# Kernel optimization log

Measured on AMD Instinct MI355X. Metric: run time of the kernel, lower is better.

The kernel has to match this reference:

```python
import jax, jax.numpy as jnp
import numpy as np

N = 100000
D = 100
E = 1600000


def setup_inputs() -> dict:
    key = jax.random.key(0)
    k1, k2, k3, k4 = jax.random.split(key, 4)
    embedding = jax.random.normal(k1, (N, D), dtype=jnp.float32)
    adj_rows = jax.random.randint(k2, (E,), 0, N, dtype=jnp.int32)
    adj_cols = jax.random.randint(k3, (E,), 0, N, dtype=jnp.int32)
    adj_vals = jax.random.uniform(k4, (E,), dtype=jnp.float32)
    return {
        "embedding": embedding,
        "adj_rows": adj_rows,
        "adj_cols": adj_cols,
        "adj_vals": adj_vals,
        "layer_num": 3,
    }


def _spmm(rows, cols, vals, x):
    # sparse [N,N] @ dense [N,D] via gather + weighted segment-sum scatter
    msgs = x[cols] * vals[:, None]           # [E, D]
    return jax.ops.segment_sum(msgs, rows, num_segments=N)  # [N, D]


def reference(embedding, adj_rows, adj_cols, adj_vals, layer_num):
    # out = sum_{i=0}^{layer_num} A^i x  (accumulate hops, including layer 0)
    h = embedding
    acc = embedding
    for _ in range(layer_num):
        h = _spmm(adj_rows, adj_cols, adj_vals, h)
        acc = acc + h
    return acc
```

## Files before the change

kernel.cpp:

```cpp
#include <hip/hip_runtime.h>


#define NODES 100000
#define DIM 100
#define DIM4 25
#define CH 16
#define BSHIFT 8
#define NBUCKETS ((NODES + 255) >> 8)
#define NPAD (NBUCKETS << BSHIFT)

typedef _Float16 half4_t __attribute__((ext_vector_type(4)));
typedef _Float16 half8_t __attribute__((ext_vector_type(8)));

__global__ void cvt_hist_kernel(const float4* __restrict__ emb, half4_t* __restrict__ x0,
                                const int* __restrict__ rows, int* __restrict__ bktCount, int E) {
    __shared__ int h[NBUCKETS];
    for (int i = threadIdx.x; i < NBUCKETS; i += blockDim.x) h[i] = 0;
    __syncthreads();
    int stride = gridDim.x * blockDim.x;
    int gid = blockIdx.x * blockDim.x + threadIdx.x;
    for (int i = gid; i < NODES * 32; i += stride) {
        int r = i >> 5, c = i & 31;
        half4_t hv;
        if (c < 25) {
            float4 f = emb[r * 25 + c];
            hv.x = (_Float16)f.x; hv.y = (_Float16)f.y;
            hv.z = (_Float16)f.z; hv.w = (_Float16)f.w;
        } else {
            hv.x = (_Float16)0.f; hv.y = (_Float16)0.f;
            hv.z = (_Float16)0.f; hv.w = (_Float16)0.f;
        }
        x0[i] = hv;
    }
    for (int e = gid; e < E; e += stride)
        atomicAdd(&h[rows[e] >> BSHIFT], 1);
    __syncthreads();
    for (int i = threadIdx.x; i < NBUCKETS; i += blockDim.x)
        if (h[i]) atomicAdd(&bktCount[i], h[i]);
}

__global__ void pass1_kernel(const int* __restrict__ rows, const int* __restrict__ cols,
                             const float* __restrict__ vals,
                             const int* __restrict__ bktCount, int* __restrict__ gCur,
                             int* __restrict__ bktStart,
                             int2* __restrict__ staging, int E) {
    __shared__ int cnt[NBUCKETS];
    __shared__ int bst[NBUCKETS];
    __shared__ int sc[512];
    int t = threadIdx.x;
    for (int i = t; i < NBUCKETS; i += 512) cnt[i] = 0;
    __syncthreads();
    int chunk = (E + gridDim.x - 1) / gridDim.x;
    int s = blockIdx.x * chunk;
    int e = min(E, s + chunk);
    for (int i = s + t; i < e; i += 512)
        atomicAdd(&cnt[rows[i] >> BSHIFT], 1);
    int v = (t < NBUCKETS) ? bktCount[t] : 0;
    sc[t] = v;
    __syncthreads();
    for (int off = 1; off < 512; off <<= 1) {
        int x = (t >= off) ? sc[t - off] : 0;
        __syncthreads();
        sc[t] += x;
        __syncthreads();
    }
    int excl = sc[t] - v;
    if (blockIdx.x == 0) {
        if (t < NBUCKETS) bktStart[t] = excl;
        if (t == 0) bktStart[NBUCKETS] = E;
    }
    if (t < NBUCKETS) {
        int c = cnt[t];
        bst[t] = excl + (c ? atomicAdd(&gCur[t], c) : 0);
        cnt[t] = 0;
    }
    __syncthreads();
    for (int i = s + t; i < e; i += 512) {
        int r = rows[i];
        int b = r >> BSHIFT;
        int pos = bst[b] + atomicAdd(&cnt[b], 1);
        staging[pos] = make_int2(cols[i] | ((r & 255) << 17), __float_as_int(vals[i]));
    }
}

__global__ void pass2_kernel(const int* __restrict__ bktStart, const int2* __restrict__ staging,
                             int* __restrict__ rowstart, int2* __restrict__ csr) {
    __shared__ int hist[256];
    __shared__ int cur[256];
    int b = blockIdx.x, t = threadIdx.x;
    int s = bktStart[b], e = bktStart[b + 1];
    if (t < 256) hist[t] = 0;
    __syncthreads();
    for (int i = s + t; i < e; i += 512)
        atomicAdd(&hist[(staging[i].x >> 17) & 255], 1);
    __syncthreads();
    int v = (t < 256) ? hist[t] : 0;
    if (t < 256) cur[t] = v;
    __syncthreads();
    for (int off = 1; off < 256; off <<= 1) {
        int x = (t >= off && t < 256) ? cur[t - off] : 0;
        __syncthreads();
        if (t < 256) cur[t] += x;
        __syncthreads();
    }
    if (t < 256) {
        int excl = cur[t] - v;
        rowstart[(b << BSHIFT) + t] = s + excl;
        hist[t] = excl;
    }
    __syncthreads();
    for (int i = s + t; i < e; i += 512) {
        int2 rec = staging[i];
        int lr = (rec.x >> 17) & 255;
        int p = atomicAdd(&hist[lr], 1);
        csr[s + p] = make_int2(rec.x & 0x1FFFF, rec.y);
    }
}

__global__ void gather_mid4_kernel(const int* __restrict__ rowstart,
                                   const int2* __restrict__ csr,
                                   const half8_t* __restrict__ x,
                                   half8_t* __restrict__ h) {
    int gid = blockIdx.x * blockDim.x + threadIdx.x;
    int row = gid >> 4, lane = gid & 15;
    if (row >= NODES) return;
    int s = rowstart[row], e = rowstart[row + 1];
    float acc[8] = {0.f, 0.f, 0.f, 0.f, 0.f, 0.f, 0.f, 0.f};
    int i = s;
    for (; i + 3 < e; i += 4) {
        int2 r0 = csr[i], r1 = csr[i + 1], r2 = csr[i + 2], r3 = csr[i + 3];
        half8_t a0 = x[((size_t)r0.x << 4) + lane];
        half8_t a1 = x[((size_t)r1.x << 4) + lane];
        half8_t a2 = x[((size_t)r2.x << 4) + lane];
        half8_t a3 = x[((size_t)r3.x << 4) + lane];
        float v0 = __int_as_float(r0.y), v1 = __int_as_float(r1.y);
        float v2 = __int_as_float(r2.y), v3 = __int_as_float(r3.y);
        #pragma unroll
        for (int k = 0; k < 8; ++k)
            acc[k] += v0 * (float)a0[k] + v1 * (float)a1[k]
                    + v2 * (float)a2[k] + v3 * (float)a3[k];
    }
    for (; i < e; ++i) {
        int2 r0 = csr[i];
        half8_t a0 = x[((size_t)r0.x << 4) + lane];
        float v0 = __int_as_float(r0.y);
        #pragma unroll
        for (int k = 0; k < 8; ++k) acc[k] += v0 * (float)a0[k];
    }
    half8_t hv;
    #pragma unroll
    for (int k = 0; k < 8; ++k) hv[k] = (_Float16)acc[k];
    h[((size_t)row << 4) + lane] = hv;
}

__global__ void gather_mid8_kernel(const int* __restrict__ rowstart,
                                   const int2* __restrict__ csr,
                                   const half8_t* __restrict__ x,
                                   half8_t* __restrict__ h) {
    int gid = blockIdx.x * blockDim.x + threadIdx.x;
    int row = gid >> 4, lane = gid & 15;
    if (row >= NODES) return;
    int s = rowstart[row], e = rowstart[row + 1];
    float acc[8] = {0.f, 0.f, 0.f, 0.f, 0.f, 0.f, 0.f, 0.f};
    int i = s;
    for (; i + 7 < e; i += 8) {
        int2 rr[8];
        #pragma unroll
        for (int j = 0; j < 8; ++j) rr[j] = csr[i + j];
        half8_t aa[8];
        #pragma unroll
        for (int j = 0; j < 8; ++j) aa[j] = x[((size_t)rr[j].x << 4) + lane];
        #pragma unroll
        for (int j = 0; j < 8; ++j) {
            float v = __int_as_float(rr[j].y);
            #pragma unroll
            for (int k = 0; k < 8; ++k) acc[k] += v * (float)aa[j][k];
        }
    }
    for (; i < e; ++i) {
        int2 r0 = csr[i];
        half8_t a0 = x[((size_t)r0.x << 4) + lane];
        float v0 = __int_as_float(r0.y);
        #pragma unroll
        for (int k = 0; k < 8; ++k) acc[k] += v0 * (float)a0[k];
    }
    half8_t hv;
    #pragma unroll
    for (int k = 0; k < 8; ++k) hv[k] = (_Float16)acc[k];
    h[((size_t)row << 4) + lane] = hv;
}

__global__ void gather_last_kernel(const int* __restrict__ rowstart,
                                   const int2* __restrict__ csr,
                                   const half8_t* __restrict__ x,
                                   const half8_t* __restrict__ x0,
                                   const half8_t* __restrict__ h1,
                                   const half8_t* __restrict__ h2,
                                   float4* __restrict__ out) {
    int gid = blockIdx.x * blockDim.x + threadIdx.x;
    int row = gid >> 4, lane = gid & 15;
    if (row >= NODES) return;
    int s = rowstart[row], e = rowstart[row + 1];
    float acc[8] = {0.f, 0.f, 0.f, 0.f, 0.f, 0.f, 0.f, 0.f};
    int i = s;
    for (; i + 7 < e; i += 8) {
        int2 rr[8];
        #pragma unroll
        for (int j = 0; j < 8; ++j) rr[j] = csr[i + j];
        half8_t aa[8];
        #pragma unroll
        for (int j = 0; j < 8; ++j) aa[j] = x[((size_t)rr[j].x << 4) + lane];
        #pragma unroll
        for (int j = 0; j < 8; ++j) {
            float v = __int_as_float(rr[j].y);
            #pragma unroll
            for (int k = 0; k < 8; ++k) acc[k] += v * (float)aa[j][k];
        }
    }
    for (; i < e; ++i) {
        int2 r0 = csr[i];
        half8_t a0 = x[((size_t)r0.x << 4) + lane];
        float v0 = __int_as_float(r0.y);
        #pragma unroll
        for (int k = 0; k < 8; ++k) acc[k] += v0 * (float)a0[k];
    }
    size_t pidx = ((size_t)row << 4) + lane;
    half8_t xe = x0[pidx], a1 = h1[pidx], a2 = h2[pidx];
    int f4 = row * DIM4 + lane * 2;
    if (lane < 13) {
        float4 o0;
        o0.x = acc[0] + (float)xe[0] + (float)a1[0] + (float)a2[0];
        o0.y = acc[1] + (float)xe[1] + (float)a1[1] + (float)a2[1];
        o0.z = acc[2] + (float)xe[2] + (float)a1[2] + (float)a2[2];
        o0.w = acc[3] + (float)xe[3] + (float)a1[3] + (float)a2[3];
        out[f4] = o0;
    }
    if (lane < 12) {
        float4 o1;
        o1.x = acc[4] + (float)xe[4] + (float)a1[4] + (float)a2[4];
        o1.y = acc[5] + (float)xe[5] + (float)a1[5] + (float)a2[5];
        o1.z = acc[6] + (float)xe[6] + (float)a1[6] + (float)a2[6];
        o1.w = acc[7] + (float)xe[7] + (float)a1[7] + (float)a2[7];
        out[f4 + 1] = o1;
    }
}

extern "C" void kernel_launch(void* const* d_in, const int* in_sizes, int n_in,
                              void* d_out, int out_size, void* d_ws, size_t ws_size,
                              hipStream_t stream) {
    const float* emb  = (const float*)d_in[0];
    const int*   rows = (const int*)  d_in[1];
    const int*   cols = (const int*)  d_in[2];
    const float* vals = (const float*)d_in[3];
    const int E = in_sizes[1];

    const size_t ndp_bytes = (size_t)NODES * 128 * sizeof(_Float16);

    char* w = (char*)d_ws;
    half8_t* x0p      = (half8_t*)w;  w += ndp_bytes;
    half8_t* h1p      = (half8_t*)w;  w += ndp_bytes;
    half8_t* h2p      = (half8_t*)w;  w += ndp_bytes;
    int2*    staging  = (int2*)h2p;
    int2*    csr      = (int2*)   w;  w += (size_t)E * sizeof(int2);
    int*     rowstart = (int*)    w;  w += (size_t)(NPAD + 256) * sizeof(int);
    int*     bktCount = (int*)    w;  w += 512 * sizeof(int);
    int*     gCur     = (int*)    w;  w += 512 * sizeof(int);
    int*     bktStart = (int*)    w;  w += 512 * sizeof(int);

    float4* out = (float4*)d_out;

    hipMemsetAsync(bktCount, 0, 1024 * sizeof(int), stream);
    cvt_hist_kernel<<<1024, 256, 0, stream>>>((const float4*)emb, (half4_t*)x0p,
                                              rows, bktCount, E);
    pass1_kernel<<<256, 512, 0, stream>>>(rows, cols, vals, bktCount, gCur, bktStart,
                                          staging, E);
    pass2_kernel<<<NBUCKETS, 512, 0, stream>>>(bktStart, staging, rowstart, csr);

    const long long threads = (long long)NODES * 16;
    dim3 gGrid((unsigned)((threads + 255) / 256)), gBlock(256);
    gather_mid4_kernel<<<gGrid, gBlock, 0, stream>>>(rowstart, csr, x0p, h1p);
    gather_mid8_kernel<<<gGrid, gBlock, 0, stream>>>(rowstart, csr, h1p, h2p);
    gather_last_kernel<<<gGrid, gBlock, 0, stream>>>(rowstart, csr, h2p, x0p, h1p, h2p, out);
}
```

Before: 363.4 us.

## Sort rows by degree within buckets and use nontemporal CSR loads in gathers

The CSR build now also produces a per-bucket permutation that groups rows by degree (counting sort on min(degree,63)). The gather kernels then read each row through this permutation, so that rows handled by neighbouring 16-lane groups in a wavefront have similar edge counts and less time is lost to divergence. CSR edge records and the x0/h1 reads in the final kernel use nontemporal loads to reduce cache pollution, and the first hop now uses the 8-way unrolled gather instead of the 4-way one. The cost is an extra permutation array and more shared-memory work in pass2, plus row writes and rowstart reads that are no longer contiguous.

```diff
diff --git a/kernel.cpp b/kernel.cpp
--- a/kernel.cpp
+++ b/kernel.cpp
@@ -11,6 +11,7 @@
 
 typedef _Float16 half4_t __attribute__((ext_vector_type(4)));
 typedef _Float16 half8_t __attribute__((ext_vector_type(8)));
+typedef int i2_raw __attribute__((ext_vector_type(2)));
 
 __global__ void cvt_hist_kernel(const float4* __restrict__ emb, half4_t* __restrict__ x0,
                                 const int* __restrict__ rows, int* __restrict__ bktCount, int E) {
@@ -84,18 +85,25 @@
 }
 
 __global__ void pass2_kernel(const int* __restrict__ bktStart, const int2* __restrict__ staging,
-                             int* __restrict__ rowstart, int2* __restrict__ csr) {
+                             int* __restrict__ rowstart, int2* __restrict__ csr,
+                             int* __restrict__ perm) {
     __shared__ int hist[256];
     __shared__ int cur[256];
+    __shared__ int dh[64];
+    __shared__ int dc[64];
+    __shared__ int dcur[64];
     int b = blockIdx.x, t = threadIdx.x;
     int s = bktStart[b], e = bktStart[b + 1];
     if (t < 256) hist[t] = 0;
+    if (t < 64) dh[t] = 0;
     __syncthreads();
     for (int i = s + t; i < e; i += 512)
         atomicAdd(&hist[(staging[i].x >> 17) & 255], 1);
     __syncthreads();
     int v = (t < 256) ? hist[t] : 0;
     if (t < 256) cur[t] = v;
+    int dbin = min(v, 63);
+    if (t < 256) atomicAdd(&dh[dbin], 1);
     __syncthreads();
     for (int off = 1; off < 256; off <<= 1) {
         int x = (t >= off && t < 256) ? cur[t - off] : 0;
@@ -107,6 +115,20 @@
         int excl = cur[t] - v;
         rowstart[(b << BSHIFT) + t] = s + excl;
         hist[t] = excl;
+    }
+    if (t < 64) dc[t] = dh[t];
+    __syncthreads();
+    for (int off = 1; off < 64; off <<= 1) {
+        int x = (t >= off && t < 64) ? dc[t - off] : 0;
+        __syncthreads();
+        if (t < 64) dc[t] += x;
+        __syncthreads();
+    }
+    if (t < 64) dcur[t] = dc[t] - dh[t];
+    __syncthreads();
+    if (t < 256) {
+        int pos = atomicAdd(&dcur[dbin], 1);
+        perm[(b << BSHIFT) + pos] = (b << BSHIFT) + t;
     }
     __syncthreads();
     for (int i = s + t; i < e; i += 512) {
@@ -117,70 +139,37 @@
     }
 }
 
-__global__ void gather_mid4_kernel(const int* __restrict__ rowstart,
-                                   const int2* __restrict__ csr,
+__global__ void gather_mid8_kernel(const int* __restrict__ rowstart,
+                                   const i2_raw* __restrict__ csr,
+                                   const int* __restrict__ perm,
                                    const half8_t* __restrict__ x,
                                    half8_t* __restrict__ h) {
     int gid = blockIdx.x * blockDim.x + threadIdx.x;
-    int row = gid >> 4, lane = gid & 15;
-    if (row >= NODES) return;
-    int s = rowstart[row], e = rowstart[row + 1];
-    float acc[8] = {0.f, 0.f, 0.f, 0.f, 0.f, 0.f, 0.f, 0.f};
-    int i = s;
-    for (; i + 3 < e; i += 4) {
-        int2 r0 = csr[i], r1 = csr[i + 1], r2 = csr[i + 2], r3 = csr[i + 3];
-        half8_t a0 = x[((size_t)r0.x << 4) + lane];
-        half8_t a1 = x[((size_t)r1.x << 4) + lane];
-        half8_t a2 = x[((size_t)r2.x << 4) + lane];
-        half8_t a3 = x[((size_t)r3.x << 4) + lane];
-        float v0 = __int_as_float(r0.y), v1 = __int_as_float(r1.y);
-        float v2 = __int_as_float(r2.y), v3 = __int_as_float(r3.y);
-        #pragma unroll
-        for (int k = 0; k < 8; ++k)
-            acc[k] += v0 * (float)a0[k] + v1 * (float)a1[k]
-                    + v2 * (float)a2[k] + v3 * (float)a3[k];
-    }
-    for (; i < e; ++i) {
-        int2 r0 = csr[i];
-        half8_t a0 = x[((size_t)r0.x << 4) + lane];
-        float v0 = __int_as_float(r0.y);
-        #pragma unroll
-        for (int k = 0; k < 8; ++k) acc[k] += v0 * (float)a0[k];
-    }
-    half8_t hv;
-    #pragma unroll
-    for (int k = 0; k < 8; ++k) hv[k] = (_Float16)acc[k];
-    h[((size_t)row << 4) + lane] = hv;
-}
-
-__global__ void gather_mid8_kernel(const int* __restrict__ rowstart,
-                                   const int2* __restrict__ csr,
-                                   const half8_t* __restrict__ x,
-                                   half8_t* __restrict__ h) {
-    int gid = blockIdx.x * blockDim.x + threadIdx.x;
-    int row = gid >> 4, lane = gid & 15;
+    int slot = gid >> 4, lane = gid & 15;
+    if (slot >= NPAD) return;
+    int row = perm[slot];
     if (row >= NODES) return;
     int s = rowstart[row], e = rowstart[row + 1];
     float acc[8] = {0.f, 0.f, 0.f, 0.f, 0.f, 0.f, 0.f, 0.f};
     int i = s;
     for (; i + 7 < e; i += 8) {
-        int2 rr[8];
-        #pragma unroll
-        for (int j = 0; j < 8; ++j) rr[j] = csr[i + j];
+        i2_raw rr[8];
+        #pragma unroll
+        for (int j = 0; j < 8; ++j) rr[j] = __builtin_nontemporal_load(&csr[i + j]);
         half8_t aa[8];
         #pragma unroll
-        for (int j = 0; j < 8; ++j) aa[j] = x[((size_t)rr[j].x << 4) + lane];
+        for (int j = 0; j < 8; ++j) aa[j] = x[((size_t)rr[j][0] << 4) + lane];
         #pragma unroll
         for (int j = 0; j < 8; ++j) {
-            float v = __int_as_float(rr[j].y);
+            float v = __int_as_float(rr[j][1]);
             #pragma unroll
             for (int k = 0; k < 8; ++k) acc[k] += v * (float)aa[j][k];
         }
     }
     for (; i < e; ++i) {
-        int2 r0 = csr[i];
-        half8_t a0 = x[((size_t)r0.x << 4) + lane];
-        float v0 = __int_as_float(r0.y);
+        i2_raw r0 = __builtin_nontemporal_load(&csr[i]);
+        half8_t a0 = x[((size_t)r0[0] << 4) + lane];
+        float v0 = __int_as_float(r0[1]);
         #pragma unroll
         for (int k = 0; k < 8; ++k) acc[k] += v0 * (float)a0[k];
     }
@@ -191,41 +180,46 @@
 }
 
 __global__ void gather_last_kernel(const int* __restrict__ rowstart,
-                                   const int2* __restrict__ csr,
+                                   const i2_raw* __restrict__ csr,
+                                   const int* __restrict__ perm,
                                    const half8_t* __restrict__ x,
                                    const half8_t* __restrict__ x0,
                                    const half8_t* __restrict__ h1,
                                    const half8_t* __restrict__ h2,
                                    float4* __restrict__ out) {
     int gid = blockIdx.x * blockDim.x + threadIdx.x;
-    int row = gid >> 4, lane = gid & 15;
+    int slot = gid >> 4, lane = gid & 15;
+    if (slot >= NPAD) return;
+    int row = perm[slot];
     if (row >= NODES) return;
     int s = rowstart[row], e = rowstart[row + 1];
     float acc[8] = {0.f, 0.f, 0.f, 0.f, 0.f, 0.f, 0.f, 0.f};
     int i = s;
     for (; i + 7 < e; i += 8) {
-        int2 rr[8];
-        #pragma unroll
-        for (int j = 0; j < 8; ++j) rr[j] = csr[i + j];
+        i2_raw rr[8];
+        #pragma unroll
+        for (int j = 0; j < 8; ++j) rr[j] = __builtin_nontemporal_load(&csr[i + j]);
         half8_t aa[8];
         #pragma unroll
-        for (int j = 0; j < 8; ++j) aa[j] = x[((size_t)rr[j].x << 4) + lane];
+        for (int j = 0; j < 8; ++j) aa[j] = x[((size_t)rr[j][0] << 4) + lane];
         #pragma unroll
         for (int j = 0; j < 8; ++j) {
-            float v = __int_as_float(rr[j].y);
+            float v = __int_as_float(rr[j][1]);
             #pragma unroll
             for (int k = 0; k < 8; ++k) acc[k] += v * (float)aa[j][k];
         }
     }
     for (; i < e; ++i) {
-        int2 r0 = csr[i];
-        half8_t a0 = x[((size_t)r0.x << 4) + lane];
-        float v0 = __int_as_float(r0.y);
+        i2_raw r0 = __builtin_nontemporal_load(&csr[i]);
+        half8_t a0 = x[((size_t)r0[0] << 4) + lane];
+        float v0 = __int_as_float(r0[1]);
         #pragma unroll
         for (int k = 0; k < 8; ++k) acc[k] += v0 * (float)a0[k];
     }
     size_t pidx = ((size_t)row << 4) + lane;
-    half8_t xe = x0[pidx], a1 = h1[pidx], a2 = h2[pidx];
+    half8_t xe = __builtin_nontemporal_load(&x0[pidx]);
+    half8_t a1 = __builtin_nontemporal_load(&h1[pidx]);
+    half8_t a2 = h2[pidx];
     int f4 = row * DIM4 + lane * 2;
     if (lane < 13) {
         float4 o0;
@@ -263,6 +257,7 @@
     int2*    staging  = (int2*)h2p;
     int2*    csr      = (int2*)   w;  w += (size_t)E * sizeof(int2);
     int*     rowstart = (int*)    w;  w += (size_t)(NPAD + 256) * sizeof(int);
+    int*     perm     = (int*)    w;  w += (size_t)NPAD * sizeof(int);
     int*     bktCount = (int*)    w;  w += 512 * sizeof(int);
     int*     gCur     = (int*)    w;  w += 512 * sizeof(int);
     int*     bktStart = (int*)    w;  w += 512 * sizeof(int);
@@ -274,11 +269,14 @@
                                               rows, bktCount, E);
     pass1_kernel<<<256, 512, 0, stream>>>(rows, cols, vals, bktCount, gCur, bktStart,
                                           staging, E);
-    pass2_kernel<<<NBUCKETS, 512, 0, stream>>>(bktStart, staging, rowstart, csr);
-
-    const long long threads = (long long)NODES * 16;
+    pass2_kernel<<<NBUCKETS, 512, 0, stream>>>(bktStart, staging, rowstart, csr, perm);
+
+    const long long threads = (long long)NPAD * 16;
     dim3 gGrid((unsigned)((threads + 255) / 256)), gBlock(256);
-    gather_mid4_kernel<<<gGrid, gBlock, 0, stream>>>(rowstart, csr, x0p, h1p);
-    gather_mid8_kernel<<<gGrid, gBlock, 0, stream>>>(rowstart, csr, h1p, h2p);
-    gather_last_kernel<<<gGrid, gBlock, 0, stream>>>(rowstart, csr, h2p, x0p, h1p, h2p, out);
-}
+    gather_mid8_kernel<<<gGrid, gBlock, 0, stream>>>(rowstart, (const i2_raw*)csr, perm,
+                                                     x0p, h1p);
+    gather_mid8_kernel<<<gGrid, gBlock, 0, stream>>>(rowstart, (const i2_raw*)csr, perm,
+                                                     h1p, h2p);
+    gather_last_kernel<<<gGrid, gBlock, 0, stream>>>(rowstart, (const i2_raw*)csr, perm,
+                                                     h2p, x0p, h1p, h2p, out);
+}
```

New measurement: 434.9 us. +19.7%, slower.

## Replace two-pass bucketed CSR build with per-row count and direct atomic scatter

Applied to the files above, without the earlier changes.

The CSR build no longer sorts edges into 256-row buckets through a staging buffer and then reorders within each bucket. It now counts edges per row with global atomics during the histogram pass, scans the counts per bucket to get row starts, and scatters each edge straight to its final slot with a per-row global atomic cursor. This drops one full pass over the edge list and the staging traffic, at the cost of many contended global atomics and scattered 8-byte writes. The first hop also switches from the 4-way-unrolled gather to the 8-way one.

```diff
diff --git a/kernel.cpp b/kernel.cpp
--- a/kernel.cpp
+++ b/kernel.cpp
@@ -13,7 +13,8 @@
 typedef _Float16 half8_t __attribute__((ext_vector_type(8)));
 
 __global__ void cvt_hist_kernel(const float4* __restrict__ emb, half4_t* __restrict__ x0,
-                                const int* __restrict__ rows, int* __restrict__ bktCount, int E) {
+                                const int* __restrict__ rows, int* __restrict__ rowCnt,
+                                int* __restrict__ bktCount, int E) {
     __shared__ int h[NBUCKETS];
     for (int i = threadIdx.x; i < NBUCKETS; i += blockDim.x) h[i] = 0;
     __syncthreads();
@@ -32,29 +33,23 @@
         }
         x0[i] = hv;
     }
-    for (int e = gid; e < E; e += stride)
-        atomicAdd(&h[rows[e] >> BSHIFT], 1);
+    for (int e = gid; e < E; e += stride) {
+        int r = rows[e];
+        atomicAdd(&rowCnt[r], 1);
+        atomicAdd(&h[r >> BSHIFT], 1);
+    }
     __syncthreads();
     for (int i = threadIdx.x; i < NBUCKETS; i += blockDim.x)
         if (h[i]) atomicAdd(&bktCount[i], h[i]);
 }
 
-__global__ void pass1_kernel(const int* __restrict__ rows, const int* __restrict__ cols,
-                             const float* __restrict__ vals,
-                             const int* __restrict__ bktCount, int* __restrict__ gCur,
-                             int* __restrict__ bktStart,
-                             int2* __restrict__ staging, int E) {
-    __shared__ int cnt[NBUCKETS];
-    __shared__ int bst[NBUCKETS];
+__global__ void rowstart_kernel(const int* __restrict__ bktCount,
+                                const int* __restrict__ rowCnt,
+                                int* __restrict__ rowstart) {
     __shared__ int sc[512];
-    int t = threadIdx.x;
-    for (int i = t; i < NBUCKETS; i += 512) cnt[i] = 0;
-    __syncthreads();
-    int chunk = (E + gridDim.x - 1) / gridDim.x;
-    int s = blockIdx.x * chunk;
-    int e = min(E, s + chunk);
-    for (int i = s + t; i < e; i += 512)
-        atomicAdd(&cnt[rows[i] >> BSHIFT], 1);
+    __shared__ int rs[256];
+    __shared__ int sbase;
+    int b = blockIdx.x, t = threadIdx.x;
     int v = (t < NBUCKETS) ? bktCount[t] : 0;
     sc[t] = v;
     __syncthreads();
@@ -64,93 +59,30 @@
         sc[t] += x;
         __syncthreads();
     }
-    int excl = sc[t] - v;
-    if (blockIdx.x == 0) {
-        if (t < NBUCKETS) bktStart[t] = excl;
-        if (t == 0) bktStart[NBUCKETS] = E;
-    }
-    if (t < NBUCKETS) {
-        int c = cnt[t];
-        bst[t] = excl + (c ? atomicAdd(&gCur[t], c) : 0);
-        cnt[t] = 0;
-    }
-    __syncthreads();
-    for (int i = s + t; i < e; i += 512) {
+    if (t == b) sbase = sc[t] - v;
+    int rv = (t < 256) ? rowCnt[(b << BSHIFT) + t] : 0;
+    if (t < 256) rs[t] = rv;
+    __syncthreads();
+    for (int off = 1; off < 256; off <<= 1) {
+        int x = (t >= off && t < 256) ? rs[t - off] : 0;
+        __syncthreads();
+        if (t < 256) rs[t] += x;
+        __syncthreads();
+    }
+    if (t < 256) rowstart[(b << BSHIFT) + t] = sbase + rs[t] - rv;
+}
+
+__global__ void scatter_kernel(const int* __restrict__ rows, const int* __restrict__ cols,
+                               const float* __restrict__ vals,
+                               const int* __restrict__ rowstart, int* __restrict__ rowCur,
+                               int2* __restrict__ csr, int E) {
+    int gid = blockIdx.x * blockDim.x + threadIdx.x;
+    int stride = gridDim.x * blockDim.x;
+    for (int i = gid; i < E; i += stride) {
         int r = rows[i];
-        int b = r >> BSHIFT;
-        int pos = bst[b] + atomicAdd(&cnt[b], 1);
-        staging[pos] = make_int2(cols[i] | ((r & 255) << 17), __float_as_int(vals[i]));
-    }
-}
-
-__global__ void pass2_kernel(const int* __restrict__ bktStart, const int2* __restrict__ staging,
-                             int* __restrict__ rowstart, int2* __restrict__ csr) {
-    __shared__ int hist[256];
-    __shared__ int cur[256];
-    int b = blockIdx.x, t = threadIdx.x;
-    int s = bktStart[b], e = bktStart[b + 1];
-    if (t < 256) hist[t] = 0;
-    __syncthreads();
-    for (int i = s + t; i < e; i += 512)
-        atomicAdd(&hist[(staging[i].x >> 17) & 255], 1);
-    __syncthreads();
-    int v = (t < 256) ? hist[t] : 0;
-    if (t < 256) cur[t] = v;
-    __syncthreads();
-    for (int off = 1; off < 256; off <<= 1) {
-        int x = (t >= off && t < 256) ? cur[t - off] : 0;
-        __syncthreads();
-        if (t < 256) cur[t] += x;
-        __syncthreads();
-    }
-    if (t < 256) {
-        int excl = cur[t] - v;
-        rowstart[(b << BSHIFT) + t] = s + excl;
-        hist[t] = excl;
-    }
-    __syncthreads();
-    for (int i = s + t; i < e; i += 512) {
-        int2 rec = staging[i];
-        int lr = (rec.x >> 17) & 255;
-        int p = atomicAdd(&hist[lr], 1);
-        csr[s + p] = make_int2(rec.x & 0x1FFFF, rec.y);
-    }
-}
-
-__global__ void gather_mid4_kernel(const int* __restrict__ rowstart,
-                                   const int2* __restrict__ csr,
-                                   const half8_t* __restrict__ x,
-                                   half8_t* __restrict__ h) {
-    int gid = blockIdx.x * blockDim.x + threadIdx.x;
-    int row = gid >> 4, lane = gid & 15;
-    if (row >= NODES) return;
-    int s = rowstart[row], e = rowstart[row + 1];
-    float acc[8] = {0.f, 0.f, 0.f, 0.f, 0.f, 0.f, 0.f, 0.f};
-    int i = s;
-    for (; i + 3 < e; i += 4) {
-        int2 r0 = csr[i], r1 = csr[i + 1], r2 = csr[i + 2], r3 = csr[i + 3];
-        half8_t a0 = x[((size_t)r0.x << 4) + lane];
-        half8_t a1 = x[((size_t)r1.x << 4) + lane];
-        half8_t a2 = x[((size_t)r2.x << 4) + lane];
-        half8_t a3 = x[((size_t)r3.x << 4) + lane];
-        float v0 = __int_as_float(r0.y), v1 = __int_as_float(r1.y);
-        float v2 = __int_as_float(r2.y), v3 = __int_as_float(r3.y);
-        #pragma unroll
-        for (int k = 0; k < 8; ++k)
-            acc[k] += v0 * (float)a0[k] + v1 * (float)a1[k]
-                    + v2 * (float)a2[k] + v3 * (float)a3[k];
-    }
-    for (; i < e; ++i) {
-        int2 r0 = csr[i];
-        half8_t a0 = x[((size_t)r0.x << 4) + lane];
-        float v0 = __int_as_float(r0.y);
-        #pragma unroll
-        for (int k = 0; k < 8; ++k) acc[k] += v0 * (float)a0[k];
-    }
-    half8_t hv;
-    #pragma unroll
-    for (int k = 0; k < 8; ++k) hv[k] = (_Float16)acc[k];
-    h[((size_t)row << 4) + lane] = hv;
+        int p = rowstart[r] + atomicAdd(&rowCur[r], 1);
+        csr[p] = make_int2(cols[i], __float_as_int(vals[i]));
+    }
 }
 
 __global__ void gather_mid8_kernel(const int* __restrict__ rowstart,
@@ -260,25 +192,23 @@
     half8_t* x0p      = (half8_t*)w;  w += ndp_bytes;
     half8_t* h1p      = (half8_t*)w;  w += ndp_bytes;
     half8_t* h2p      = (half8_t*)w;  w += ndp_bytes;
-    int2*    staging  = (int2*)h2p;
     int2*    csr      = (int2*)   w;  w += (size_t)E * sizeof(int2);
-    int*     rowstart = (int*)    w;  w += (size_t)(NPAD + 256) * sizeof(int);
+    int*     rowstart = (int*)    w;  w += (size_t)(NPAD + 8) * sizeof(int);
+    int*     rowCnt   = (int*)    w;  w += (size_t)NPAD * sizeof(int);
+    int*     rowCur   = (int*)    w;  w += (size_t)NPAD * sizeof(int);
     int*     bktCount = (int*)    w;  w += 512 * sizeof(int);
-    int*     gCur     = (int*)    w;  w += 512 * sizeof(int);
-    int*     bktStart = (int*)    w;  w += 512 * sizeof(int);
 
     float4* out = (float4*)d_out;
 
-    hipMemsetAsync(bktCount, 0, 1024 * sizeof(int), stream);
+    hipMemsetAsync(rowCnt, 0, (size_t)(2 * NPAD + 512) * sizeof(int), stream);
     cvt_hist_kernel<<<1024, 256, 0, stream>>>((const float4*)emb, (half4_t*)x0p,
-                                              rows, bktCount, E);
-    pass1_kernel<<<256, 512, 0, stream>>>(rows, cols, vals, bktCount, gCur, bktStart,
-                                          staging, E);
-    pass2_kernel<<<NBUCKETS, 512, 0, stream>>>(bktStart, staging, rowstart, csr);
+                                              rows, rowCnt, bktCount, E);
+    rowstart_kernel<<<NBUCKETS, 512, 0, stream>>>(bktCount, rowCnt, rowstart);
+    scatter_kernel<<<2048, 256, 0, stream>>>(rows, cols, vals, rowstart, rowCur, csr, E);
 
     const long long threads = (long long)NODES * 16;
     dim3 gGrid((unsigned)((threads + 255) / 256)), gBlock(256);
-    gather_mid4_kernel<<<gGrid, gBlock, 0, stream>>>(rowstart, csr, x0p, h1p);
+    gather_mid8_kernel<<<gGrid, gBlock, 0, stream>>>(rowstart, csr, x0p, h1p);
     gather_mid8_kernel<<<gGrid, gBlock, 0, stream>>>(rowstart, csr, h1p, h2p);
     gather_last_kernel<<<gGrid, gBlock, 0, stream>>>(rowstart, csr, h2p, x0p, h1p, h2p, out);
 }
```

Result: slower. 478.7 us (+31.7%).

## Reuse per-block bucket histograms from cvt_hist to skip recount in pass1

Applied to the files above, without the earlier changes.

The histogram kernel now counts edges over contiguous per-block chunks and writes each block's per-bucket counts to a workspace array. pass1 reads those counts instead of rereading rows and doing a second shared-memory atomic histogram. Both kernels use the same 512-block chunking so the counts line up. The cost is an extra global array write and read, plus fewer blocks for the conversion loop in cvt_hist.

```diff
diff --git a/kernel.cpp b/kernel.cpp
--- a/kernel.cpp
+++ b/kernel.cpp
@@ -8,12 +8,14 @@
 #define BSHIFT 8
 #define NBUCKETS ((NODES + 255) >> 8)
 #define NPAD (NBUCKETS << BSHIFT)
+#define NCHUNK 512
 
 typedef _Float16 half4_t __attribute__((ext_vector_type(4)));
 typedef _Float16 half8_t __attribute__((ext_vector_type(8)));
 
 __global__ void cvt_hist_kernel(const float4* __restrict__ emb, half4_t* __restrict__ x0,
-                                const int* __restrict__ rows, int* __restrict__ bktCount, int E) {
+                                const int* __restrict__ rows, int* __restrict__ blkCnt,
+                                int* __restrict__ bktCount, int E) {
     __shared__ int h[NBUCKETS];
     for (int i = threadIdx.x; i < NBUCKETS; i += blockDim.x) h[i] = 0;
     __syncthreads();
@@ -32,29 +34,27 @@
         }
         x0[i] = hv;
     }
-    for (int e = gid; e < E; e += stride)
-        atomicAdd(&h[rows[e] >> BSHIFT], 1);
-    __syncthreads();
-    for (int i = threadIdx.x; i < NBUCKETS; i += blockDim.x)
+    int chunk = (E + gridDim.x - 1) / gridDim.x;
+    int s = blockIdx.x * chunk;
+    int e = min(E, s + chunk);
+    for (int i = s + threadIdx.x; i < e; i += blockDim.x)
+        atomicAdd(&h[rows[i] >> BSHIFT], 1);
+    __syncthreads();
+    for (int i = threadIdx.x; i < NBUCKETS; i += blockDim.x) {
+        blkCnt[blockIdx.x * NBUCKETS + i] = h[i];
         if (h[i]) atomicAdd(&bktCount[i], h[i]);
+    }
 }
 
 __global__ void pass1_kernel(const int* __restrict__ rows, const int* __restrict__ cols,
                              const float* __restrict__ vals,
-                             const int* __restrict__ bktCount, int* __restrict__ gCur,
-                             int* __restrict__ bktStart,
+                             const int* __restrict__ bktCount, const int* __restrict__ blkCnt,
+                             int* __restrict__ gCur, int* __restrict__ bktStart,
                              int2* __restrict__ staging, int E) {
     __shared__ int cnt[NBUCKETS];
     __shared__ int bst[NBUCKETS];
     __shared__ int sc[512];
     int t = threadIdx.x;
-    for (int i = t; i < NBUCKETS; i += 512) cnt[i] = 0;
-    __syncthreads();
-    int chunk = (E + gridDim.x - 1) / gridDim.x;
-    int s = blockIdx.x * chunk;
-    int e = min(E, s + chunk);
-    for (int i = s + t; i < e; i += 512)
-        atomicAdd(&cnt[rows[i] >> BSHIFT], 1);
     int v = (t < NBUCKETS) ? bktCount[t] : 0;
     sc[t] = v;
     __syncthreads();
@@ -70,11 +70,14 @@
         if (t == 0) bktStart[NBUCKETS] = E;
     }
     if (t < NBUCKETS) {
-        int c = cnt[t];
+        int c = blkCnt[blockIdx.x * NBUCKETS + t];
         bst[t] = excl + (c ? atomicAdd(&gCur[t], c) : 0);
         cnt[t] = 0;
     }
     __syncthreads();
+    int chunk = (E + gridDim.x - 1) / gridDim.x;
+    int s = blockIdx.x * chunk;
+    int e = min(E, s + chunk);
     for (int i = s + t; i < e; i += 512) {
         int r = rows[i];
         int b = r >> BSHIFT;
@@ -266,14 +269,15 @@
     int*     bktCount = (int*)    w;  w += 512 * sizeof(int);
     int*     gCur     = (int*)    w;  w += 512 * sizeof(int);
     int*     bktStart = (int*)    w;  w += 512 * sizeof(int);
+    int*     blkCnt   = (int*)    w;  w += (size_t)NCHUNK * NBUCKETS * sizeof(int);
 
     float4* out = (float4*)d_out;
 
     hipMemsetAsync(bktCount, 0, 1024 * sizeof(int), stream);
-    cvt_hist_kernel<<<1024, 256, 0, stream>>>((const float4*)emb, (half4_t*)x0p,
-                                              rows, bktCount, E);
-    pass1_kernel<<<256, 512, 0, stream>>>(rows, cols, vals, bktCount, gCur, bktStart,
-                                          staging, E);
+    cvt_hist_kernel<<<NCHUNK, 256, 0, stream>>>((const float4*)emb, (half4_t*)x0p,
+                                                rows, blkCnt, bktCount, E);
+    pass1_kernel<<<NCHUNK, 512, 0, stream>>>(rows, cols, vals, bktCount, blkCnt,
+                                             gCur, bktStart, staging, E);
     pass2_kernel<<<NBUCKETS, 512, 0, stream>>>(bktStart, staging, rowstart, csr);
 
     const long long threads = (long long)NODES * 16;
```

After: 366.0 us. Within noise of the previous version (+0.7%).
